# Optimization experiments

Measured on AMD Instinct MI355X. Metric: run time of the kernel, lower is better.

The kernel has to match this reference:

```python
import jax, jax.numpy as jnp
import numpy as np

B, S, D, F = 4, 4096, 512, 2048
EPS = 1e-5


def _layer_norm(x, g, b):
    # LayerNorm((sqlength, mdim)): normalize jointly over last two dims
    mu = jnp.mean(x, axis=(-2, -1), keepdims=True)
    var = jnp.mean(jnp.square(x - mu), axis=(-2, -1), keepdims=True)
    return (x - mu) * jax.lax.rsqrt(var + EPS) * g + b


def _attn(q, k, v, causal):
    # scores: [B, S_q, S_k]
    s = jnp.einsum('bqd,bkd->bqk', q, k) / jnp.sqrt(jnp.asarray(D, q.dtype))
    if causal:
        mask = jnp.triu(jnp.ones((s.shape[-2], s.shape[-1]), dtype=bool), k=1)
        s = jnp.where(mask, -jnp.inf, s)
    p = jax.nn.softmax(s, axis=-1)
    return jnp.einsum('bqk,bkd->bqd', p, v)


def setup_inputs() -> dict:
    key = jax.random.key(0)
    ks = jax.random.split(key, 12)
    sc = 0.02
    return {
        'x':    jax.random.normal(ks[0], (B, S, D), jnp.float32),
        'enc':  jax.random.normal(ks[1], (B, S, D), jnp.float32),
        'Wo1':  jax.random.normal(ks[2], (D, D), jnp.float32) * sc,
        'Wo2':  jax.random.normal(ks[3], (D, D), jnp.float32) * sc,
        'ln1_g': jnp.ones((S, D), jnp.float32),
        'ln1_b': jnp.zeros((S, D), jnp.float32),
        'ln2_g': jnp.ones((S, D), jnp.float32),
        'ln2_b': jnp.zeros((S, D), jnp.float32),
        'W1':   jax.random.normal(ks[4], (F, D), jnp.float32) * sc,
        'b1':   jnp.zeros((F,), jnp.float32),
        'W2':   jax.random.normal(ks[5], (D, F), jnp.float32) * sc,
        'b2':   jnp.zeros((D,), jnp.float32),
    }


def reference(x, enc, Wo1, Wo2, ln1_g, ln1_b, ln2_g, ln2_b, W1, b1, W2, b2):
    # 1) causal self-attention + residual + ln1
    o = _attn(x, x, x, causal=True) @ Wo1.T
    x = _layer_norm(o + x, ln1_g, ln1_b)
    # 2) cross attention (q=enc, k=enc, v=x per source) + residual + ln2
    o = _attn(enc, enc, x, causal=False) @ Wo2.T
    x = _layer_norm(o + x, ln2_g, ln2_b)
    # 3) position-wise FFN (original looped per token; vectorized here) + residual + ln2 (shared params)
    ff = jax.nn.relu(x @ W1.T + b1) @ W2.T + b2
    return _layer_norm(ff + x, ln2_g, ln2_b)
```

## Files before the change

kernel.cpp:

```cpp
#include <hip/hip_runtime.h>
#include <cstdint>
#include <cstddef>

#define NB 4
#define NS 4096
#define ND 512
#define NF 2048

typedef __bf16 bf16;
typedef __attribute__((ext_vector_type(8))) __bf16 bf16x8;
typedef __attribute__((ext_vector_type(4))) __bf16 bf16x4;
typedef __attribute__((ext_vector_type(4))) float f32x4;

#define MFMA16(a, b, c) __builtin_amdgcn_mfma_f32_16x16x32_bf16((a), (b), (c), 0, 0, 0)

__device__ __forceinline__ void async_copy16(void* lds, const void* g) {
  __builtin_amdgcn_global_load_lds(
      (__attribute__((address_space(1))) unsigned int*)(uintptr_t)g,
      (__attribute__((address_space(3))) unsigned int*)(unsigned)(uintptr_t)lds,
      16, 0, 0);
}

__device__ __forceinline__ int vswz_col(int c , int dloc) {
  return (c & ~31) | (((((c >> 3) & 3) + ((dloc >> 1) & 3)) & 3) << 3);
}

__global__ void k_detect(const unsigned short* __restrict__ x, unsigned* __restrict__ flag) {
  __shared__ int cnt;
  if (threadIdx.x == 0) cnt = 0;
  __syncthreads();
  int bad = 0;
  for (int i = threadIdx.x; i < 2048; i += 256) {
    unsigned e = (x[i] >> 7) & 0xFF;
    if (e < 100 || e > 140) bad++;
  }
  atomicAdd(&cnt, bad);
  __syncthreads();
  if (threadIdx.x == 0) *flag = (cnt > 200) ? 1u : 0u;
}

__global__ void k_norm_bf16(const void* __restrict__ src, bf16* __restrict__ dst,
                            const unsigned* __restrict__ flag, int n) {
  int i = (blockIdx.x * 256 + threadIdx.x) * 8;
  if (i >= n) return;
  if (*flag) {
    const float* s = (const float*)src;
    float4 a = *(const float4*)(s + i);
    float4 c = *(const float4*)(s + i + 4);
    bf16x8 v;
    v[0] = (bf16)a.x; v[1] = (bf16)a.y; v[2] = (bf16)a.z; v[3] = (bf16)a.w;
    v[4] = (bf16)c.x; v[5] = (bf16)c.y; v[6] = (bf16)c.z; v[7] = (bf16)c.w;
    *(bf16x8*)(dst + i) = v;
  } else {
    *(uint4*)(dst + i) = *(const uint4*)((const bf16*)src + i);
  }
}

__global__ void k_norm_f32(const void* __restrict__ src, float* __restrict__ dst,
                           const unsigned* __restrict__ flag, int n) {
  int i = blockIdx.x * 256 + threadIdx.x;
  if (i >= n) return;
  dst[i] = (*flag) ? ((const float*)src)[i] : (float)((const bf16*)src)[i];
}

__global__ void k_transpose(const bf16* __restrict__ in, bf16* __restrict__ out) {
  __shared__ bf16 t[64][72];
  const int b = blockIdx.z, s0 = blockIdx.x * 64, d0 = blockIdx.y * 64;
  const int tid = threadIdx.x;
#pragma unroll
  for (int it = 0; it < 2; ++it) {
    int slot = it * 256 + tid;
    int r = slot >> 3, c = (slot & 7) * 8;
    *(bf16x8*)&t[r][c] = *(const bf16x8*)&in[((size_t)b * NS + s0 + r) * ND + d0 + c];
  }
  __syncthreads();
#pragma unroll
  for (int it = 0; it < 2; ++it) {
    int slot = it * 256 + tid;
    int r = slot >> 3, c = (slot & 7) * 8;
    bf16x8 v;
#pragma unroll
    for (int k = 0; k < 8; ++k) v[k] = t[c + k][r];
    *(bf16x8*)&out[((size_t)b * ND + d0 + r) * NS + s0 + vswz_col(c, r)] = v;
  }
}

template <bool CAUSAL>
__global__ __launch_bounds__(512, 2) void k_attn8(const bf16* __restrict__ Q,
                                                  const bf16* __restrict__ Km,
                                                  const bf16* __restrict__ Vt,
                                                  bf16* __restrict__ O0, bf16* __restrict__ O1,
                                                  float2* __restrict__ ml) {
  __shared__ bf16 lds_[65536];

  const int tid = threadIdx.x;
  const int w = tid >> 6, lane = tid & 63, quad = lane >> 4, l15 = lane & 15;
  const int slot = blockIdx.x & 7;
  const int b = slot >> 1;
  const int z = slot & 1;
  const int j = (int)(blockIdx.x >> 3);

  int qwb, nLo, n;
  if (CAUSAL) {
    nLo = j + 1;
    n = 65;
    qwb = (w < 4) ? (64 * j + w * 16) : (4032 - 64 * j + (w - 4) * 16);
  } else {
    nLo = 1 << 30;
    n = 64;
    qwb = j * 128 + w * 16;
  }
  const int nHi = 64 - j;

  const bf16* Kg = Km + (size_t)b * NS * ND;
  const bf16* Vg = Vt + (size_t)b * ND * NS;

  auto ktOf = [&](int i) -> int {
    if (!CAUSAL) return z * 64 + i;
    return (i < nLo) ? (z * nLo + i) : (z * nHi + (i - nLo));
  };

  const bf16* Qg = Q + ((size_t)b * NS + qwb + l15) * ND;
  bf16x8 qf[16];
#pragma unroll
  for (int s = 0; s < 16; ++s) qf[s] = *(const bf16x8*)&Qg[s * 32 + quad * 8];
#pragma unroll
  for (int s = 0; s < 16; ++s)
#pragma unroll
    for (int jj = 0; jj < 8; ++jj) qf[s][jj] = (bf16)((float)qf[s][jj] * 0.044194173824159216f);

  f32x4 o[32];
#pragma unroll
  for (int i = 0; i < 32; ++i) o[i] = (f32x4){0.f, 0.f, 0.f, 0.f};

  float m = -1e30f, l = 0.f;

  const int laneA4 = ((((quad * 2) & 3) * 16) + l15) * 4;
  const int laneB4 = ((((quad * 2 + 1) & 3) * 16) + l15) * 4;
  const int vsw = ((quad + ((l15 >> 1) & 3)) & 3) * 8;

  auto STAGE = [&](bf16* base, int k0) {
#pragma unroll
    for (int i = 0; i < 4; ++i) {
      const int r = w * 4 + i;
      const int g = (lane & ~7) | ((lane ^ r) & 7);
      async_copy16(base + r * 512, Kg + (size_t)(k0 + r) * ND + g * 8);
    }
#pragma unroll
    for (int i = 0; i < 4; ++i) {
      const int d0 = (w * 4 + i) * 16;
      async_copy16(base + 16384 + d0 * 32, Vg + (size_t)(d0 + (lane >> 2)) * NS + k0 + (lane & 3) * 8);
    }
  };

  int buf = 0;
  STAGE(lds_, ktOf(0) * 32);
  __syncthreads();

  for (int i = 0; i < n; ++i) {
    const int k0 = ktOf(i) * 32;
    bf16* Ks = lds_ + buf * 32768;
    bf16* Vs = Ks + 16384;
    if (i + 1 < n) STAGE(lds_ + (buf ^ 1) * 32768, ktOf(i + 1) * 32);

    const bool active = !CAUSAL || ((w >= 4) == (i >= nLo));
    if (active) {
      f32x4 sa0 = (f32x4){0.f, 0.f, 0.f, 0.f};
      f32x4 sa1 = (f32x4){0.f, 0.f, 0.f, 0.f};
      __builtin_amdgcn_s_setprio(1);
#pragma unroll
      for (int s = 0; s < 16; ++s) {
        const int lc = s * 4 + quad;
        const int swz = ((lc & ~7) | ((lc ^ l15) & 7)) * 8;
        bf16x8 a0 = *(const bf16x8*)&Ks[l15 * 512 + swz];
        bf16x8 a1 = *(const bf16x8*)&Ks[(16 + l15) * 512 + swz];
        sa0 = MFMA16(a0, qf[s], sa0);
        sa1 = MFMA16(a1, qf[s], sa1);
      }
      __builtin_amdgcn_s_setprio(0);

      float sv[8];
      {
        const int qrow = qwb + l15;
        const bool needMask = CAUSAL && (k0 + 31 > qwb);
#pragma unroll
        for (int kt2 = 0; kt2 < 2; ++kt2)
#pragma unroll
          for (int r = 0; r < 4; ++r) {
            float s = (kt2 == 0) ? sa0[r] : sa1[r];
            if (needMask) {
              int key = k0 + kt2 * 16 + quad * 4 + r;
              if (key > qrow) s = -1e30f;
            }
            sv[kt2 * 4 + r] = s;
          }
      }
      float tm = sv[0];
#pragma unroll
      for (int i2 = 1; i2 < 8; ++i2) tm = fmaxf(tm, sv[i2]);
      tm = fmaxf(tm, __shfl_xor(tm, 16));
      tm = fmaxf(tm, __shfl_xor(tm, 32));
      const float mn = fmaxf(m, tm);
      const float alpha = __expf(m - mn);
      m = mn;
      float pf[8];
      float ts = 0.f;
#pragma unroll
      for (int i2 = 0; i2 < 8; ++i2) { pf[i2] = __expf(sv[i2] - mn); ts += pf[i2]; }
      ts += __shfl_xor(ts, 16);
      ts += __shfl_xor(ts, 32);
      l = l * alpha + ts;
      if (__ballot(alpha < 0.99999f)) {
#pragma unroll
        for (int dt = 0; dt < 32; ++dt)
#pragma unroll
          for (int r = 0; r < 4; ++r) o[dt][r] *= alpha;
      }

      bf16x8 pb;
#pragma unroll
      for (int jj = 0; jj < 8; ++jj) {
        const int r_ = jj & 3;
        const int sl = (jj < 4) ? laneA4 : laneB4;
        float v0 = __int_as_float(__builtin_amdgcn_ds_bpermute(sl, __float_as_int(pf[r_])));
        float v1 = __int_as_float(__builtin_amdgcn_ds_bpermute(sl, __float_as_int(pf[4 + r_])));
        pb[jj] = (bf16)(quad < 2 ? v0 : v1);
      }

      __builtin_amdgcn_s_setprio(1);
#pragma unroll
      for (int dt = 0; dt < 32; ++dt) {
        bf16x8 a = *(const bf16x8*)&Vs[(dt * 16 + l15) * 32 + vsw];
        o[dt] = MFMA16(a, pb, o[dt]);
      }
      __builtin_amdgcn_s_setprio(0);
    }

    __syncthreads();
    buf ^= 1;
  }

  const float inv = 1.f / l;
  if (lane < 16 && quad == 0) ml[((size_t)z * NB + b) * NS + qwb + lane] = make_float2(m, l);
  bf16* Ow = lds_ + w * 8192;
#pragma unroll
  for (int dt = 0; dt < 32; ++dt) {
    bf16x4 v;
#pragma unroll
    for (int r = 0; r < 4; ++r) v[r] = (bf16)(o[dt][r] * inv);
    *(bf16x4*)&Ow[l15 * 512 + dt * 16 + quad * 4] = v;
  }
  bf16* Og = (z ? O1 : O0) + ((size_t)b * NS + qwb) * ND;
#pragma unroll
  for (int it = 0; it < 16; ++it) {
    bf16x8 row = *(const bf16x8*)&Ow[it * 512 + lane * 8];
    *(bf16x8*)&Og[(size_t)it * ND + lane * 8] = row;
  }
}

__global__ void k_merge(bf16* __restrict__ O0, const bf16* __restrict__ O1,
                        const float2* __restrict__ ml) {
  size_t i = ((size_t)blockIdx.x * 256 + threadIdx.x) * 8;
  int row = (int)(i >> 9);
  float2 a = ml[row];
  float2 c = ml[(size_t)NB * NS + row];
  float M = fmaxf(a.x, c.x);
  float w0 = __expf(a.x - M) * a.y;
  float w1 = __expf(c.x - M) * c.y;
  float den = 1.f / (w0 + w1);
  float c0 = w0 * den, c1 = w1 * den;
  bf16x8 v0 = *(const bf16x8*)(O0 + i);
  bf16x8 v1 = *(const bf16x8*)(O1 + i);
  bf16x8 ov;
#pragma unroll
  for (int k = 0; k < 8; ++k) ov[k] = (bf16)(c0 * (float)v0[k] + c1 * (float)v1[k]);
  *(bf16x8*)(O0 + i) = ov;
}

template <int RES_MODE, bool HAS_BIAS, bool RELU, bool STATS>
__global__ __launch_bounds__(256) void k_gemm(const bf16* __restrict__ A, const bf16* __restrict__ W,
                                              const bf16* __restrict__ resid,
                                              const float* __restrict__ bias, bf16* __restrict__ Out,
                                              float* __restrict__ stats, int M, int N, int K,
                                              int rowOfs) {
  __shared__ bf16 As[128 * 64];
  __shared__ bf16 Ws[128 * 64];
  const int tid = threadIdx.x;
  const int w = tid >> 6, lane = tid & 63, quad = lane >> 4, l15 = lane & 15;
  const int m0 = blockIdx.x * 128, n0 = blockIdx.y * 128;
  const int wr = (w >> 1) * 64, wc = (w & 1) * 64;
  const int arow = lane >> 3, acol = (lane & 7) * 8;

  f32x4 acc[16];
#pragma unroll
  for (int i = 0; i < 16; ++i) acc[i] = (f32x4){0.f, 0.f, 0.f, 0.f};

  for (int k0 = 0; k0 < K; k0 += 64) {
    __syncthreads();
#pragma unroll
    for (int i = 0; i < 4; ++i) {
      const int rbase = (w * 4 + i) * 8 + arow;
      async_copy16(&As[(w * 4 + i) * 512], A + (size_t)(m0 + rbase) * K + k0 + acol);
      async_copy16(&Ws[(w * 4 + i) * 512], W + (size_t)(n0 + rbase) * K + k0 + acol);
    }
    __syncthreads();
#pragma unroll
    for (int s = 0; s < 2; ++s) {
      bf16x8 af[4], bw[4];
#pragma unroll
      for (int i = 0; i < 4; ++i) af[i] = *(const bf16x8*)&As[(wr + i * 16 + l15) * 64 + s * 32 + quad * 8];
#pragma unroll
      for (int jj = 0; jj < 4; ++jj) bw[jj] = *(const bf16x8*)&Ws[(wc + jj * 16 + l15) * 64 + s * 32 + quad * 8];
#pragma unroll
      for (int i = 0; i < 4; ++i)
#pragma unroll
        for (int jj = 0; jj < 4; ++jj) acc[i * 4 + jj] = MFMA16(af[i], bw[jj], acc[i * 4 + jj]);
    }
  }

  float lsum = 0.f, lsq = 0.f;
#pragma unroll
  for (int i = 0; i < 4; ++i)
#pragma unroll
    for (int jj = 0; jj < 4; ++jj)
#pragma unroll
      for (int r = 0; r < 4; ++r) {
        int row = m0 + wr + i * 16 + quad * 4 + r;
        int col = n0 + wc + jj * 16 + l15;
        float v = acc[i * 4 + jj][r];
        if (HAS_BIAS) v += bias[col];
        if (RELU) v = fmaxf(v, 0.f);
        if (RES_MODE == 2) v += (float)resid[(size_t)row * N + col];
        Out[(size_t)row * N + col] = (bf16)v;
        if (STATS) { lsum += v; lsq += v * v; }
      }

  if (STATS) {
    __syncthreads();
    float* red = (float*)As;
    red[tid] = lsum;
    red[256 + tid] = lsq;
    __syncthreads();
    for (int off = 128; off > 0; off >>= 1) {
      if (tid < off) { red[tid] += red[tid + off]; red[256 + tid] += red[256 + tid + off]; }
      __syncthreads();
    }
    if (tid == 0) {
      int bidx = (rowOfs + m0) >> 12;
      atomicAdd(&stats[bidx * 2], red[0]);
      atomicAdd(&stats[bidx * 2 + 1], red[256]);
    }
  }
}

template <bool FINAL>
__global__ void k_ln(const bf16* __restrict__ T, const float* __restrict__ stats,
                     const void* __restrict__ gp, const void* __restrict__ bp,
                     void* __restrict__ outp, const unsigned* __restrict__ flag) {
  const float invN = 1.f / 2097152.f;
  size_t i = ((size_t)(blockIdx.x * 256 + threadIdx.x)) * 8;
  int b = (int)(i >> 21);
  int sd = (int)(i & 2097151);
  float mu = stats[b * 2] * invN;
  float var = stats[b * 2 + 1] * invN - mu * mu;
  float rs = rsqrtf(var + 1e-5f);
  bool f32m = (*flag != 0);
  bf16x8 tv = *(const bf16x8*)(T + i);
  float gv[8], bv[8];
  if (f32m) {
    float4 a = *(const float4*)((const float*)gp + sd), c = *(const float4*)((const float*)gp + sd + 4);
    gv[0] = a.x; gv[1] = a.y; gv[2] = a.z; gv[3] = a.w; gv[4] = c.x; gv[5] = c.y; gv[6] = c.z; gv[7] = c.w;
    float4 e = *(const float4*)((const float*)bp + sd), f = *(const float4*)((const float*)bp + sd + 4);
    bv[0] = e.x; bv[1] = e.y; bv[2] = e.z; bv[3] = e.w; bv[4] = f.x; bv[5] = f.y; bv[6] = f.z; bv[7] = f.w;
  } else {
    bf16x8 g8 = *(const bf16x8*)((const bf16*)gp + sd);
    bf16x8 b8 = *(const bf16x8*)((const bf16*)bp + sd);
#pragma unroll
    for (int k = 0; k < 8; ++k) { gv[k] = (float)g8[k]; bv[k] = (float)b8[k]; }
  }
  float ov[8];
#pragma unroll
  for (int k = 0; k < 8; ++k) ov[k] = ((float)tv[k] - mu) * rs * gv[k] + bv[k];
  if (FINAL && f32m) {
    float4 o0 = {ov[0], ov[1], ov[2], ov[3]}, o1 = {ov[4], ov[5], ov[6], ov[7]};
    *(float4*)((float*)outp + i) = o0;
    *(float4*)((float*)outp + i + 4) = o1;
  } else {
    bf16x8 o8;
#pragma unroll
    for (int k = 0; k < 8; ++k) o8[k] = (bf16)ov[k];
    *(bf16x8*)((bf16*)outp + i) = o8;
  }
}

__global__ void k_ln_t(const bf16* __restrict__ T, const float* __restrict__ stats,
                       const void* __restrict__ gp, const void* __restrict__ bp,
                       bf16* __restrict__ X, bf16* __restrict__ XT,
                       const unsigned* __restrict__ flag) {
  __shared__ bf16 t[64][72];
  const float invN = 1.f / 2097152.f;
  const int b = blockIdx.z, s0 = blockIdx.x * 64, d0 = blockIdx.y * 64;
  const int tid = threadIdx.x;
  const float mu = stats[b * 2] * invN;
  const float var = stats[b * 2 + 1] * invN - mu * mu;
  const float rs = rsqrtf(var + 1e-5f);
  const bool f32m = (*flag != 0);
#pragma unroll
  for (int it = 0; it < 2; ++it) {
    int slot = it * 256 + tid;
    int r = slot >> 3, c = (slot & 7) * 8;
    size_t idx = ((size_t)b * NS + s0 + r) * ND + d0 + c;
    size_t pidx = (size_t)(s0 + r) * ND + d0 + c;
    bf16x8 tv = *(const bf16x8*)&T[idx];
    float gv[8], bv[8];
    if (f32m) {
      float4 a = *(const float4*)((const float*)gp + pidx), cc = *(const float4*)((const float*)gp + pidx + 4);
      gv[0] = a.x; gv[1] = a.y; gv[2] = a.z; gv[3] = a.w; gv[4] = cc.x; gv[5] = cc.y; gv[6] = cc.z; gv[7] = cc.w;
      float4 e = *(const float4*)((const float*)bp + pidx), f = *(const float4*)((const float*)bp + pidx + 4);
      bv[0] = e.x; bv[1] = e.y; bv[2] = e.z; bv[3] = e.w; bv[4] = f.x; bv[5] = f.y; bv[6] = f.z; bv[7] = f.w;
    } else {
      bf16x8 g8 = *(const bf16x8*)((const bf16*)gp + pidx);
      bf16x8 b8 = *(const bf16x8*)((const bf16*)bp + pidx);
#pragma unroll
      for (int k = 0; k < 8; ++k) { gv[k] = (float)g8[k]; bv[k] = (float)b8[k]; }
    }
    bf16x8 ov;
#pragma unroll
    for (int k = 0; k < 8; ++k) ov[k] = (bf16)(((float)tv[k] - mu) * rs * gv[k] + bv[k]);
    *(bf16x8*)&X[idx] = ov;
    *(bf16x8*)&t[r][c] = ov;
  }
  __syncthreads();
#pragma unroll
  for (int it = 0; it < 2; ++it) {
    int slot = it * 256 + tid;
    int r = slot >> 3, c = (slot & 7) * 8;
    bf16x8 v;
#pragma unroll
    for (int k = 0; k < 8; ++k) v[k] = t[c + k][r];
    *(bf16x8*)&XT[((size_t)b * ND + d0 + r) * NS + s0 + vswz_col(c, r)] = v;
  }
}

extern "C" void kernel_launch(void* const* d_in, const int* in_sizes, int n_in, void* d_out,
                              int out_size, void* d_ws, size_t ws_size, hipStream_t stream) {
  (void)in_sizes; (void)n_in; (void)out_size;
  const void* x_raw = d_in[0];
  const void* enc_raw = d_in[1];
  const void* Wo1_raw = d_in[2];
  const void* Wo2_raw = d_in[3];
  const void* g1_raw = d_in[4];
  const void* bb1_raw = d_in[5];
  const void* g2_raw = d_in[6];
  const void* bb2_raw = d_in[7];
  const void* W1_raw = d_in[8];
  const void* bias1_raw = d_in[9];
  const void* W2_raw = d_in[10];
  const void* bias2_raw = d_in[11];

  char* w = (char*)d_ws;
  unsigned* flag = (unsigned*)(w + 0);
  float* stats = (float*)(w + 16);
  float* b1f = (float*)(w + 1024);
  float* b2f = (float*)(w + 1024 + 8192);
  size_t off = 16384;
  const size_t nBSD = (size_t)NB * NS * ND;
  bf16* Wo1b = (bf16*)(w + off); off += (size_t)ND * ND * 2;
  bf16* Wo2b = (bf16*)(w + off); off += (size_t)ND * ND * 2;
  bf16* W1b = (bf16*)(w + off); off += (size_t)NF * ND * 2;
  bf16* W2b = (bf16*)(w + off); off += (size_t)ND * NF * 2;
  bf16* xb = (bf16*)(w + off); off += nBSD * 2;
  bf16* Ab = (bf16*)(w + off); off += nBSD * 2;
  bf16* Tb = (bf16*)(w + off); off += nBSD * 2;
  bf16* X1b = (bf16*)(w + off); off += nBSD * 2;
  bf16* Hb = (bf16*)(w + off);
  const size_t hbFull = (size_t)NB * NS * NF * 2;
  const size_t hbHalf = hbFull / 2;
  const bool ffnFull = (ws_size >= off + hbFull);
  if (!ffnFull && ws_size < off + hbHalf) return;

  bf16* O1b = Hb;
  float2* mlb = (float2*)((char*)Hb + nBSD * 2);

  hipMemsetAsync(stats, 0, 24 * sizeof(float), stream);
  k_detect<<<1, 256, 0, stream>>>((const unsigned short*)x_raw, flag);

  k_norm_bf16<<<(int)(nBSD / 2048), 256, 0, stream>>>(x_raw, xb, flag, (int)nBSD);
  k_norm_bf16<<<(ND * ND) / 2048, 256, 0, stream>>>(Wo1_raw, Wo1b, flag, ND * ND);
  k_norm_bf16<<<(ND * ND) / 2048, 256, 0, stream>>>(Wo2_raw, Wo2b, flag, ND * ND);
  k_norm_bf16<<<(NF * ND) / 2048, 256, 0, stream>>>(W1_raw, W1b, flag, NF * ND);
  k_norm_bf16<<<(NF * ND) / 2048, 256, 0, stream>>>(W2_raw, W2b, flag, ND * NF);
  k_norm_f32<<<8, 256, 0, stream>>>(bias1_raw, b1f, flag, NF);
  k_norm_f32<<<2, 256, 0, stream>>>(bias2_raw, b2f, flag, ND);

  k_transpose<<<dim3(NS / 64, ND / 64, NB), 256, 0, stream>>>(xb, Tb);
  k_attn8<true><<<256, 512, 0, stream>>>(xb, xb, Tb, Ab, O1b, mlb);
  k_merge<<<(int)(nBSD / 2048), 256, 0, stream>>>(Ab, O1b, mlb);
  k_gemm<2, false, false, true><<<dim3(128, 4), 256, 0, stream>>>(Ab, Wo1b, xb, nullptr, Tb,
                                                                  stats + 0, NB * NS, ND, ND, 0);
  k_ln_t<<<dim3(NS / 64, ND / 64, NB), 256, 0, stream>>>(Tb, stats + 0, g1_raw, bb1_raw, X1b, Ab,
                                                         flag);
  k_norm_bf16<<<(int)(nBSD / 2048), 256, 0, stream>>>(enc_raw, xb, flag, (int)nBSD);

  k_attn8<false><<<256, 512, 0, stream>>>(xb, xb, Ab, Tb, O1b, mlb);
  k_merge<<<(int)(nBSD / 2048), 256, 0, stream>>>(Tb, O1b, mlb);
  k_gemm<2, false, false, true><<<dim3(128, 4), 256, 0, stream>>>(Tb, Wo2b, X1b, nullptr, Ab,
                                                                  stats + 8, NB * NS, ND, ND, 0);
  k_ln<false><<<(int)(nBSD / 2048), 256, 0, stream>>>(Ab, stats + 8, g2_raw, bb2_raw, X1b, flag);

  const int nChunk = ffnFull ? 1 : 2;
  const int rows = ffnFull ? (NB * NS) : 8192;
  for (int c = 0; c < nChunk; ++c) {
    size_t ro = (size_t)c * rows;
    k_gemm<0, true, true, false><<<dim3(rows / 128, 16), 256, 0, stream>>>(
        X1b + ro * ND, W1b, nullptr, b1f, Hb, nullptr, rows, NF, ND, 0);
    k_gemm<2, true, false, true><<<dim3(rows / 128, 4), 256, 0, stream>>>(
        Hb, W2b, X1b + ro * ND, b2f, Tb + ro * ND, stats + 16, rows, ND, NF, (int)ro);
  }
  k_ln<true><<<(int)(nBSD / 2048), 256, 0, stream>>>(Tb, stats + 16, g2_raw, bb2_raw, d_out, flag);
}
```

Before: 783.7 us.

## Split PV across waves by head-dim slice, sharing P through LDS

The attention kernel stops giving each wave all 512 V columns for its own 16 query rows. Each wave now computes QK^T and softmax for its rows and writes bf16 P and alpha to LDS. After a barrier, every wave computes PV for a 64-wide D slice across all query slices, loading its V fragments straight from global memory into registers. K stays double-buffered in LDS while V staging is dropped. This balances PV work across waves in the causal case, where half the waves used to sit idle each step, at the cost of an extra barrier per tile and uncached global V loads.

```diff
diff --git a/kernel.cpp b/kernel.cpp
--- a/kernel.cpp
+++ b/kernel.cpp
@@ -85,13 +85,38 @@
   }
 }
 
+#define PV_HALF(QS0)                                                              \
+  {                                                                               \
+    float al_[4];                                                                 \
+    _Pragma("unroll") for (int qq = 0; qq < 4; ++qq)                              \
+        al_[qq] = alds[(QS0 + qq) * 16 + l15];                                    \
+    float amin = fminf(fminf(al_[0], al_[1]), fminf(al_[2], al_[3]));             \
+    if (__ballot(amin < 0.99999f)) {                                              \
+      _Pragma("unroll") for (int qq = 0; qq < 4; ++qq)                            \
+          _Pragma("unroll") for (int ds = 0; ds < 4; ++ds)                        \
+              _Pragma("unroll") for (int r2 = 0; r2 < 4; ++r2)                    \
+                  o[ds * 8 + QS0 + qq][r2] *= al_[qq];                            \
+    }                                                                             \
+    __builtin_amdgcn_s_setprio(1);                                                \
+    _Pragma("unroll") for (int qq = 0; qq < 4; ++qq) {                            \
+      bf16x8 pb = *(const bf16x8*)&Pt[((QS0 + qq) * 16 + l15) * 32 + quad * 8];   \
+      _Pragma("unroll") for (int ds = 0; ds < 4; ++ds)                            \
+          o[ds * 8 + QS0 + qq] = MFMA16(vr[ds], pb, o[ds * 8 + QS0 + qq]);        \
+    }                                                                             \
+    __builtin_amdgcn_s_setprio(0);                                                \
+  }
+
 template <bool CAUSAL>
-__global__ __launch_bounds__(512, 2) void k_attn8(const bf16* __restrict__ Q,
+__global__ __launch_bounds__(512, 2) void k_attn9(const bf16* __restrict__ Q,
                                                   const bf16* __restrict__ Km,
                                                   const bf16* __restrict__ Vt,
                                                   bf16* __restrict__ O0, bf16* __restrict__ O1,
                                                   float2* __restrict__ ml) {
-  __shared__ bf16 lds_[65536];
+  __shared__ __align__(16) char smem[74752];
+  bf16* Klds = (bf16*)smem;
+  bf16* Pt = (bf16*)(smem + 65536);
+  float* alds = (float*)(smem + 73728);
+  float* llds = (float*)(smem + 74240);
 
   const int tid = threadIdx.x;
   const int w = tid >> 6, lane = tid & 63, quad = lane >> 4, l15 = lane & 15;
@@ -135,36 +160,34 @@
 
   float m = -1e30f, l = 0.f;
 
-  const int laneA4 = ((((quad * 2) & 3) * 16) + l15) * 4;
-  const int laneB4 = ((((quad * 2 + 1) & 3) * 16) + l15) * 4;
   const int vsw = ((quad + ((l15 >> 1) & 3)) & 3) * 8;
 
-  auto STAGE = [&](bf16* base, int k0) {
-#pragma unroll
-    for (int i = 0; i < 4; ++i) {
-      const int r = w * 4 + i;
+  auto STAGE_K = [&](bf16* base, int k0) {
+#pragma unroll
+    for (int i2 = 0; i2 < 4; ++i2) {
+      const int r = w * 4 + i2;
       const int g = (lane & ~7) | ((lane ^ r) & 7);
       async_copy16(base + r * 512, Kg + (size_t)(k0 + r) * ND + g * 8);
     }
-#pragma unroll
-    for (int i = 0; i < 4; ++i) {
-      const int d0 = (w * 4 + i) * 16;
-      async_copy16(base + 16384 + d0 * 32, Vg + (size_t)(d0 + (lane >> 2)) * NS + k0 + (lane & 3) * 8);
-    }
   };
 
   int buf = 0;
-  STAGE(lds_, ktOf(0) * 32);
+  STAGE_K(Klds, ktOf(0) * 32);
   __syncthreads();
 
   for (int i = 0; i < n; ++i) {
     const int k0 = ktOf(i) * 32;
-    bf16* Ks = lds_ + buf * 32768;
-    bf16* Vs = Ks + 16384;
-    if (i + 1 < n) STAGE(lds_ + (buf ^ 1) * 32768, ktOf(i + 1) * 32);
-
-    const bool active = !CAUSAL || ((w >= 4) == (i >= nLo));
-    if (active) {
+    bf16* Ks = Klds + buf * 16384;
+
+    bf16x8 vr[4];
+#pragma unroll
+    for (int ds = 0; ds < 4; ++ds)
+      vr[ds] = *(const bf16x8*)&Vg[(size_t)(w * 64 + ds * 16 + l15) * NS + k0 + vsw];
+
+    if (i + 1 < n) STAGE_K(Klds + (buf ^ 1) * 16384, ktOf(i + 1) * 32);
+
+    const bool qactive = !CAUSAL || ((w >= 4) == (i >= nLo));
+    if (qactive) {
       f32x4 sa0 = (f32x4){0.f, 0.f, 0.f, 0.f};
       f32x4 sa1 = (f32x4){0.f, 0.f, 0.f, 0.f};
       __builtin_amdgcn_s_setprio(1);
@@ -210,51 +233,57 @@
       ts += __shfl_xor(ts, 16);
       ts += __shfl_xor(ts, 32);
       l = l * alpha + ts;
-      if (__ballot(alpha < 0.99999f)) {
-#pragma unroll
-        for (int dt = 0; dt < 32; ++dt)
-#pragma unroll
-          for (int r = 0; r < 4; ++r) o[dt][r] *= alpha;
+
+      bf16x4 pA, pB;
+#pragma unroll
+      for (int r2 = 0; r2 < 4; ++r2) { pA[r2] = (bf16)pf[r2]; pB[r2] = (bf16)pf[4 + r2]; }
+      *(bf16x4*)&Pt[(w * 16 + l15) * 32 + quad * 4] = pA;
+      *(bf16x4*)&Pt[(w * 16 + l15) * 32 + 16 + quad * 4] = pB;
+      if (quad == 0) alds[w * 16 + l15] = alpha;
+    }
+    __syncthreads();
+
+    if (CAUSAL) {
+      if (i >= nLo) { PV_HALF(4); } else { PV_HALF(0); }
+    } else {
+      PV_HALF(0);
+      PV_HALF(4);
+    }
+    __syncthreads();
+    buf ^= 1;
+  }
+
+  if (quad == 0) {
+    llds[w * 16 + l15] = l;
+    ml[((size_t)z * NB + b) * NS + qwb + l15] = make_float2(m, l);
+  }
+  __syncthreads();
+  bf16* EP = Klds;
+  bf16* Og = (z ? O1 : O0);
+#pragma unroll
+  for (int half = 0; half < 2; ++half) {
+#pragma unroll
+    for (int qq = 0; qq < 4; ++qq) {
+      const int qs = half * 4 + qq;
+      const float invl = 1.f / llds[qs * 16 + l15];
+#pragma unroll
+      for (int ds = 0; ds < 4; ++ds) {
+        bf16x4 v;
+#pragma unroll
+        for (int r2 = 0; r2 < 4; ++r2) v[r2] = (bf16)(o[ds * 8 + qs][r2] * invl);
+        *(bf16x4*)&EP[(qs * 16 + l15 - half * 64) * 520 + w * 64 + ds * 16 + quad * 4] = v;
       }
-
-      bf16x8 pb;
-#pragma unroll
-      for (int jj = 0; jj < 8; ++jj) {
-        const int r_ = jj & 3;
-        const int sl = (jj < 4) ? laneA4 : laneB4;
-        float v0 = __int_as_float(__builtin_amdgcn_ds_bpermute(sl, __float_as_int(pf[r_])));
-        float v1 = __int_as_float(__builtin_amdgcn_ds_bpermute(sl, __float_as_int(pf[4 + r_])));
-        pb[jj] = (bf16)(quad < 2 ? v0 : v1);
-      }
-
-      __builtin_amdgcn_s_setprio(1);
-#pragma unroll
-      for (int dt = 0; dt < 32; ++dt) {
-        bf16x8 a = *(const bf16x8*)&Vs[(dt * 16 + l15) * 32 + vsw];
-        o[dt] = MFMA16(a, pb, o[dt]);
-      }
-      __builtin_amdgcn_s_setprio(0);
-    }
-
-    __syncthreads();
-    buf ^= 1;
-  }
-
-  const float inv = 1.f / l;
-  if (lane < 16 && quad == 0) ml[((size_t)z * NB + b) * NS + qwb + lane] = make_float2(m, l);
-  bf16* Ow = lds_ + w * 8192;
-#pragma unroll
-  for (int dt = 0; dt < 32; ++dt) {
-    bf16x4 v;
-#pragma unroll
-    for (int r = 0; r < 4; ++r) v[r] = (bf16)(o[dt][r] * inv);
-    *(bf16x4*)&Ow[l15 * 512 + dt * 16 + quad * 4] = v;
-  }
-  bf16* Og = (z ? O1 : O0) + ((size_t)b * NS + qwb) * ND;
-#pragma unroll
-  for (int it = 0; it < 16; ++it) {
-    bf16x8 row = *(const bf16x8*)&Ow[it * 512 + lane * 8];
-    *(bf16x8*)&Og[(size_t)it * ND + lane * 8] = row;
+    }
+    __syncthreads();
+#pragma unroll
+    for (int r2 = 0; r2 < 8; ++r2) {
+      const int row = w * 8 + r2;
+      int qg;
+      if (CAUSAL) qg = (half == 0) ? (64 * j + row) : (4032 - 64 * j + row);
+      else qg = j * 128 + half * 64 + row;
+      *(bf16x8*)&Og[((size_t)b * NS + qg) * ND + lane * 8] = *(const bf16x8*)&EP[row * 520 + lane * 8];
+    }
+    __syncthreads();
   }
 }
 
@@ -494,7 +523,7 @@
   k_norm_f32<<<2, 256, 0, stream>>>(bias2_raw, b2f, flag, ND);
 
   k_transpose<<<dim3(NS / 64, ND / 64, NB), 256, 0, stream>>>(xb, Tb);
-  k_attn8<true><<<256, 512, 0, stream>>>(xb, xb, Tb, Ab, O1b, mlb);
+  k_attn9<true><<<256, 512, 0, stream>>>(xb, xb, Tb, Ab, O1b, mlb);
   k_merge<<<(int)(nBSD / 2048), 256, 0, stream>>>(Ab, O1b, mlb);
   k_gemm<2, false, false, true><<<dim3(128, 4), 256, 0, stream>>>(Ab, Wo1b, xb, nullptr, Tb,
                                                                   stats + 0, NB * NS, ND, ND, 0);
@@ -502,7 +531,7 @@
                                                          flag);
   k_norm_bf16<<<(int)(nBSD / 2048), 256, 0, stream>>>(enc_raw, xb, flag, (int)nBSD);
 
-  k_attn8<false><<<256, 512, 0, stream>>>(xb, xb, Ab, Tb, O1b, mlb);
+  k_attn9<false><<<256, 512, 0, stream>>>(xb, xb, Ab, Tb, O1b, mlb);
   k_merge<<<(int)(nBSD / 2048), 256, 0, stream>>>(Tb, O1b, mlb);
   k_gemm<2, false, false, true><<<dim3(128, 4), 256, 0, stream>>>(Tb, Wo2b, X1b, nullptr, Ab,
                                                                   stats + 8, NB * NS, ND, ND, 0);
```

New measurement: 1.348 ms. 1.72x slower.
